# Kernel optimization log

Measured on AMD Instinct MI355X. Metric: run time of the kernel, lower is better.

## Reference

```python
import jax, jax.numpy as jnp
import numpy as np

B, L, D = 4, 4096, 128
BLOCK, SPARSITY = 64, 0.9
NEG = -1e9


def _make_block_mask(key):
    nb = L // BLOCK
    bm = jax.random.uniform(key, (nb, nb)) > SPARSITY
    bm = bm | jnp.eye(nb, dtype=bool)  # keep diagonal blocks so no row is fully masked
    bm = jnp.tril(bm)
    return jnp.repeat(jnp.repeat(bm, BLOCK, axis=0), BLOCK, axis=1)  # [L, L]


def _xavier(key, shape):
    limit = float(np.sqrt(6.0 / (shape[0] + shape[1])))
    return jax.random.uniform(key, shape, jnp.float32, -limit, limit)


def setup_inputs() -> dict:
    key = jax.random.key(0)
    ks = jax.random.split(key, 10)
    t = lambda k: jax.random.normal(k, (B, L, D), jnp.float32)
    return {
        'q_real': t(ks[0]), 'q_imag': t(ks[1]),
        'k_real': t(ks[2]), 'k_imag': t(ks[3]),
        'v_real': t(ks[4]), 'v_imag': t(ks[5]),
        'W_qkv': _xavier(ks[6], (6 * D, 6 * D)),
        'b_qkv': jnp.zeros((6 * D,), jnp.float32),
        'W_out': _xavier(ks[7], (2 * D, 2 * D)),
        'b_out': jnp.zeros((2 * D,), jnp.float32),
        'block_mask': _make_block_mask(ks[8]),
    }


def reference(q_real, q_imag, k_real, k_imag, v_real, v_imag,
              W_qkv, b_qkv, W_out, b_out, block_mask):
    d = q_real.shape[-1]
    scale = d ** -0.5
    # fused qkv projection over the 6 concatenated channels
    x = jnp.concatenate([q_real, q_imag, k_real, k_imag, v_real, v_imag], axis=-1)  # [B,L,6D]
    qkv = (x @ W_qkv.T + b_qkv).reshape(x.shape[0], x.shape[1], 6, d)
    q_r, q_i, k_r, k_i, v_r, v_i = (qkv[:, :, j] for j in range(6))

    def attn(q, k, v):
        s = jnp.einsum('bqd,bkd->bqk', q, k) * scale          # [B,L,L]
        s = jnp.where(block_mask[None], s, NEG)               # block-sparse mask
        a = jax.nn.softmax(s, axis=-1)                        # dropout = identity (eval)
        return jnp.einsum('bqk,bkd->bqd', a, v)

    out = jnp.concatenate([attn(q_r, k_r, v_r), attn(q_i, k_i, v_i)], axis=-1)  # [B,L,2D]
    out = out @ W_out.T + b_out
    return out[..., :d], out[..., d:]
```

## Files before the change

### kernel.cpp

```cpp
#include <hip/hip_runtime.h>
#include <hip/hip_bf16.h>

typedef unsigned short u16;
typedef __attribute__((ext_vector_type(8))) short bf16x8;
typedef __attribute__((ext_vector_type(4))) float f32x4;

#define SEQ_L 4096
#define M_TOT 16384

__device__ __forceinline__ float bf2f(u16 x) {
    unsigned u = ((unsigned)x) << 16;
    return __builtin_bit_cast(float, u);
}
__device__ __forceinline__ u16 f2bf(float f) {
    unsigned u = __builtin_bit_cast(unsigned, f);
    u += 0x7FFFu + ((u >> 16) & 1u);
    return (u16)(u >> 16);
}
__device__ __forceinline__ void gload16(const u16* g, u16* l) {
    __builtin_amdgcn_global_load_lds(
        (const __attribute__((address_space(1))) unsigned int*)g,
        (__attribute__((address_space(3))) unsigned int*)l, 16, 0, 0);
}

__global__ __launch_bounds__(256) void prep_all(
    const float* __restrict__ in0, const float* __restrict__ in1, const float* __restrict__ in2,
    const float* __restrict__ in3, const float* __restrict__ in4, const float* __restrict__ in5,
    const float* __restrict__ Wqkv, const float* __restrict__ Wout, const void* __restrict__ mask,
    u16* __restrict__ x, u16* __restrict__ Wqkv_bf, u16* __restrict__ Wout_bf,
    unsigned char* __restrict__ cmask) {
    int id = blockIdx.x * 256 + threadIdx.x;
    if (id < 1572864) {
        const float* ins[6] = {in0, in1, in2, in3, in4, in5};
        int which = id >> 18, j = id & 262143;
        int m = j >> 4, c8 = j & 15;
        const float* sp = ins[which] + (size_t)m * 128 + c8 * 8;
        float4 a = *(const float4*)sp;
        float4 b = *(const float4*)(sp + 4);
        u16 t[8] = {f2bf(a.x), f2bf(a.y), f2bf(a.z), f2bf(a.w),
                    f2bf(b.x), f2bf(b.y), f2bf(b.z), f2bf(b.w)};
        *(uint4*)(x + (size_t)m * 768 + which * 128 + c8 * 8) = *(uint4*)t;
    } else if (id < 1572864 + 73728 + 8192) {
        int i = id - 1572864;
        const float* src = (i < 73728) ? Wqkv : Wout;
        u16* dst = (i < 73728) ? Wqkv_bf : Wout_bf;
        if (i >= 73728) i -= 73728;
        const float* sp = src + (size_t)i * 8;
        float4 a = *(const float4*)sp;
        float4 b = *(const float4*)(sp + 4);
        u16 t[8] = {f2bf(a.x), f2bf(a.y), f2bf(a.z), f2bf(a.w),
                    f2bf(b.x), f2bf(b.y), f2bf(b.z), f2bf(b.w)};
        *(uint4*)(dst + (size_t)i * 8) = *(uint4*)t;
    } else if (id < 1572864 + 73728 + 8192 + 4096) {
        int i = id - 1572864 - 73728 - 8192;
        int bi = i >> 6, bj = i & 63;
        size_t e = (size_t)(bi * 64) * SEQ_L + (size_t)bj * 64;
        const unsigned char* p8 = (const unsigned char*)mask;
        unsigned w0 = *(const unsigned*)mask;
        bool v;
        if (w0 == 0x01010101u || w0 == 0xFFFFFFFFu)      v = p8[e] != 0;
        else if (w0 == 0x3F803F80u || w0 == 0x3C003C00u) v = ((const u16*)mask)[e] != 0;
        else                                             v = ((const unsigned*)mask)[e] != 0;
        cmask[i] = v ? 1 : 0;
    }
}

__global__ __launch_bounds__(256, 4) void qkv_gemm(
    const u16* __restrict__ X, const u16* __restrict__ W, const float* __restrict__ bias,
    u16* __restrict__ qk, u16* __restrict__ vt) {
    __shared__ __align__(16) u16 As[128 * 64];
    __shared__ __align__(16) u16 Bs[64 * 64];
    int m0 = blockIdx.x * 128, n0 = blockIdx.y * 64;
    int tid = threadIdx.x, lane = tid & 63, w = tid >> 6;
    int ln = lane & 15, quad = lane >> 4;
    int rw = (w >> 1) * 64, cw = (w & 1) * 32;
    int lr8 = lane >> 3, lc = lane & 7;
    f32x4 acc[4][2] = {};
    for (int kk = 0; kk < 768; kk += 64) {
        __syncthreads();
        #pragma unroll
        for (int j = 0; j < 4; j++) {
            int r0 = w * 32 + j * 8, r = r0 + lr8;
            gload16(X + (size_t)(m0 + r) * 768 + kk + ((lc ^ (r & 7)) * 8), As + r0 * 64 + lane * 8);
        }
        #pragma unroll
        for (int j = 0; j < 2; j++) {
            int r0 = w * 16 + j * 8, r = r0 + lr8;
            gload16(W + (size_t)(n0 + r) * 768 + kk + ((lc ^ (r & 7)) * 8), Bs + r0 * 64 + lane * 8);
        }
        __syncthreads();
        #pragma unroll
        for (int s = 0; s < 2; s++) {
            bf16x8 af[4], bfr[2];
            #pragma unroll
            for (int i = 0; i < 4; i++) {
                int R = rw + i * 16 + ln;
                af[i] = *(const bf16x8*)(As + R * 64 + ((4 * s + quad) ^ (ln & 7)) * 8);
            }
            #pragma unroll
            for (int t = 0; t < 2; t++) {
                int R = cw + t * 16 + ln;
                bfr[t] = *(const bf16x8*)(Bs + R * 64 + ((4 * s + quad) ^ (ln & 7)) * 8);
            }
            #pragma unroll
            for (int i = 0; i < 4; i++)
                #pragma unroll
                for (int t = 0; t < 2; t++)
                    acc[i][t] = __builtin_amdgcn_mfma_f32_16x16x32_bf16(af[i], bfr[t], acc[i][t], 0, 0, 0);
        }
    }
    #pragma unroll
    for (int i = 0; i < 4; i++) {
        int row0 = m0 + rw + i * 16 + 4 * quad;
        #pragma unroll
        for (int t = 0; t < 2; t++) {
            int col = n0 + cw + t * 16 + ln;
            float bv = bias[col];
            if (col < 512) {
                #pragma unroll
                for (int r = 0; r < 4; r++)
                    qk[(size_t)(row0 + r) * 512 + col] = f2bf(acc[i][t][r] + bv);
            } else {
                int d = col - 512;
                int b = row0 >> 12, seq = row0 & 4095;
                u16 pk[4] = {f2bf(acc[i][t][0] + bv), f2bf(acc[i][t][1] + bv),
                             f2bf(acc[i][t][2] + bv), f2bf(acc[i][t][3] + bv)};
                *(ushort4*)(vt + ((size_t)(b * 2 + (d >> 7)) * 128 + (d & 127)) * SEQ_L + seq)
                    = *(ushort4*)pk;
            }
        }
    }
}

__global__ __launch_bounds__(256) void attn_out(
    const u16* __restrict__ qk, const u16* __restrict__ vt, const u16* __restrict__ Wout,
    const unsigned char* __restrict__ cmask, const float* __restrict__ bout,
    float* __restrict__ out) {
    __shared__ __align__(16) u16 Ks[2][64 * 128];
    __shared__ __align__(16) u16 Vt[2][128 * 64];
    __shared__ __align__(16) u16 PsAo[32 * 256];

    int idx = blockIdx.x;
    int qi = (idx < 256) ? (63 - (idx >> 3)) : ((idx - 256) >> 3);
    int sub = idx & 7, b = sub >> 1, half = sub & 1;
    int tid = threadIdx.x, lane = tid & 63, w = tid >> 6;
    int ln = lane & 15, quad = lane >> 4;
    int cw = w >> 1, wr = w & 1;
    const float scale = 0.08838834764831845f;

    const unsigned char* mrow = cmask + qi * 64;
    unsigned long long bm = 0;
    for (int k = 0; k <= qi; k++) bm |= (unsigned long long)(mrow[k] != 0) << k;

    const u16* kb_base = qk + (size_t)b * SEQ_L * 512 + 256 + cw * 128;
    const u16* vt_base = vt + (size_t)(b * 2 + cw) * 128 * SEQ_L;

    bf16x8 qf[4];
    {
        size_t grow = (size_t)(b * SEQ_L + qi * 64 + half * 32 + wr * 16 + ln);
        const u16* qp = qk + grow * 512 + cw * 128;
        #pragma unroll
        for (int s = 0; s < 4; s++) qf[s] = *(const bf16x8*)(qp + 32 * s + 8 * quad);
    }
    float m_st[4], l_st[4];
    #pragma unroll
    for (int r = 0; r < 4; r++) { m_st[r] = -1e30f; l_st[r] = 0.f; }
    f32x4 accO[8] = {};
    u16* Ps = PsAo + w * 1152;

    while (bm) {
        int cur = __ffsll(bm) - 1; bm &= bm - 1;
        __syncthreads();
        {
            const u16* kp = kb_base + (size_t)cur * 64 * 512;
            const u16* vp = vt_base + cur * 64;
            #pragma unroll
            for (int j = 0; j < 8; j++) {
                int kr0 = j * 8 + wr * 4, kr = kr0 + (lane >> 4);
                gload16(kp + (size_t)kr * 512 + (((lane & 15) ^ (kr & 7)) * 8),
                        Ks[cw] + kr0 * 128 + lane * 8);
                int d0 = j * 16 + wr * 8, d = d0 + (lane >> 3);
                gload16(vp + (size_t)d * SEQ_L + (((lane & 7) ^ (d & 7)) * 8),
                        Vt[cw] + d0 * 64 + lane * 8);
            }
        }
        __syncthreads();

        f32x4 accS[4] = {};
        #pragma unroll
        for (int s = 0; s < 4; s++) {
            #pragma unroll
            for (int t = 0; t < 4; t++) {
                int R = t * 16 + ln;
                bf16x8 bfr = *(const bf16x8*)(Ks[cw] + R * 128 + ((4 * s + quad) ^ (ln & 7)) * 8);
                accS[t] = __builtin_amdgcn_mfma_f32_16x16x32_bf16(qf[s], bfr, accS[t], 0, 0, 0);
            }
        }
        float P[4][4];
        #pragma unroll
        for (int r = 0; r < 4; r++) {
            float sv[4];
            float mx = -1e30f;
            #pragma unroll
            for (int t = 0; t < 4; t++) { sv[t] = accS[t][r] * scale; mx = fmaxf(mx, sv[t]); }
            #pragma unroll
            for (int off = 1; off < 16; off <<= 1) mx = fmaxf(mx, __shfl_xor(mx, off, 64));
            float nm = fmaxf(m_st[r], mx);
            float alpha = __expf(m_st[r] - nm);
            m_st[r] = nm;
            float rs = 0.f;
            #pragma unroll
            for (int t = 0; t < 4; t++) { float p = __expf(sv[t] - nm); P[t][r] = p; rs += p; }
            #pragma unroll
            for (int off = 1; off < 16; off <<= 1) rs += __shfl_xor(rs, off, 64);
            l_st[r] = l_st[r] * alpha + rs;
            #pragma unroll
            for (int nt = 0; nt < 8; nt++) accO[nt][r] *= alpha;
        }
        #pragma unroll
        for (int t = 0; t < 4; t++)
            #pragma unroll
            for (int r = 0; r < 4; r++)
                Ps[(4 * quad + r) * 72 + ln + 16 * t] = f2bf(P[t][r]);
        #pragma unroll
        for (int s2 = 0; s2 < 2; s2++) {
            bf16x8 pf = *(const bf16x8*)(Ps + ln * 72 + 32 * s2 + 8 * quad);
            #pragma unroll
            for (int nt = 0; nt < 8; nt++) {
                int R = nt * 16 + ln;
                bf16x8 vf = *(const bf16x8*)(Vt[cw] + R * 64 + ((4 * s2 + quad) ^ (ln & 7)) * 8);
                accO[nt] = __builtin_amdgcn_mfma_f32_16x16x32_bf16(pf, vf, accO[nt], 0, 0, 0);
            }
        }
    }

    __syncthreads();
    {
        float inv[4];
        #pragma unroll
        for (int r = 0; r < 4; r++) inv[r] = 1.0f / fmaxf(l_st[r], 1e-20f);
        #pragma unroll
        for (int nt = 0; nt < 8; nt++)
            #pragma unroll
            for (int r = 0; r < 4; r++)
                PsAo[(wr * 16 + 4 * quad + r) * 256 + cw * 128 + nt * 16 + ln]
                    = f2bf(accO[nt][r] * inv[r]);
    }

    u16* Bs = Ks[0];
    f32x4 oacc[2][4] = {};
    for (int kk = 0; kk < 4; kk++) {
        __syncthreads();
        #pragma unroll
        for (int j = 0; j < 8; j++) {
            int o0 = w * 64 + j * 8, o = o0 + (lane >> 3);
            gload16(Wout + (size_t)o * 256 + kk * 64 + (((lane & 7) ^ (o & 7)) * 8),
                    Bs + o0 * 64 + lane * 8);
        }
        __syncthreads();
        #pragma unroll
        for (int s = 0; s < 2; s++) {
            bf16x8 af[2], bfr[4];
            #pragma unroll
            for (int i = 0; i < 2; i++)
                af[i] = *(const bf16x8*)(PsAo + (i * 16 + ln) * 256 + kk * 64 + 32 * s + 8 * quad);
            #pragma unroll
            for (int t = 0; t < 4; t++) {
                int o = w * 64 + t * 16 + ln;
                bfr[t] = *(const bf16x8*)(Bs + o * 64 + ((4 * s + quad) ^ (ln & 7)) * 8);
            }
            #pragma unroll
            for (int i = 0; i < 2; i++)
                #pragma unroll
                for (int t = 0; t < 4; t++)
                    oacc[i][t] = __builtin_amdgcn_mfma_f32_16x16x32_bf16(af[i], bfr[t], oacc[i][t], 0, 0, 0);
        }
    }
    const size_t hlf = (size_t)M_TOT * 128;
    #pragma unroll
    for (int t = 0; t < 4; t++) {
        int o = w * 64 + t * 16 + ln;
        float bv = bout[o];
        float* base = (o < 128) ? (out + o) : (out + hlf + (o - 128));
        #pragma unroll
        for (int i = 0; i < 2; i++) {
            int row = b * SEQ_L + qi * 64 + half * 32 + i * 16 + 4 * quad;
            #pragma unroll
            for (int r = 0; r < 4; r++)
                base[(size_t)(row + r) * 128] = oacc[i][t][r] + bv;
        }
    }
}

extern "C" void kernel_launch(void* const* d_in, const int* in_sizes, int n_in,
                              void* d_out, int out_size, void* d_ws, size_t ws_size,
                              hipStream_t stream) {
    char* ws = (char*)d_ws;
    u16* x_bf    = (u16*)ws;
    u16* qk_buf  = x_bf + (size_t)M_TOT * 768;
    u16* vt_buf  = qk_buf + (size_t)M_TOT * 512;
    u16* Wqkv_bf = vt_buf + (size_t)1024 * SEQ_L;
    u16* Wout_bf = Wqkv_bf + 589824;
    unsigned char* cmask = (unsigned char*)(Wout_bf + 65536);

    hipLaunchKernelGGL(prep_all, dim3(6480), dim3(256), 0, stream,
                       (const float*)d_in[0], (const float*)d_in[1], (const float*)d_in[2],
                       (const float*)d_in[3], (const float*)d_in[4], (const float*)d_in[5],
                       (const float*)d_in[6], (const float*)d_in[8], d_in[10],
                       x_bf, Wqkv_bf, Wout_bf, cmask);
    hipLaunchKernelGGL(qkv_gemm, dim3(128, 12), dim3(256), 0, stream,
                       x_bf, Wqkv_bf, (const float*)d_in[7], qk_buf, vt_buf);
    hipLaunchKernelGGL(attn_out, dim3(512), dim3(256), 0, stream,
                       qk_buf, vt_buf, Wout_bf, cmask, (const float*)d_in[9], (float*)d_out);
}
```

Baseline: 219.0 us.

## Split attention into wave-independent sparse kernel plus separate output GEMM

```diff
diff --git a/kernel.cpp b/kernel.cpp
--- a/kernel.cpp
+++ b/kernel.cpp
@@ -28,7 +28,7 @@
     const float* __restrict__ in3, const float* __restrict__ in4, const float* __restrict__ in5,
     const float* __restrict__ Wqkv, const float* __restrict__ Wout, const void* __restrict__ mask,
     u16* __restrict__ x, u16* __restrict__ Wqkv_bf, u16* __restrict__ Wout_bf,
-    unsigned char* __restrict__ cmask) {
+    unsigned long long* __restrict__ bmap) {
     int id = blockIdx.x * 256 + threadIdx.x;
     if (id < 1572864) {
         const float* ins[6] = {in0, in1, in2, in3, in4, in5};
@@ -61,7 +61,8 @@
         if (w0 == 0x01010101u || w0 == 0xFFFFFFFFu)      v = p8[e] != 0;
         else if (w0 == 0x3F803F80u || w0 == 0x3C003C00u) v = ((const u16*)mask)[e] != 0;
         else                                             v = ((const unsigned*)mask)[e] != 0;
-        cmask[i] = v ? 1 : 0;
+        unsigned long long bits = __ballot(v);
+        if ((i & 63) == 0) bmap[bi] = bits;
     }
 }
 
@@ -132,162 +133,156 @@
     }
 }
 
-__global__ __launch_bounds__(256) void attn_out(
-    const u16* __restrict__ qk, const u16* __restrict__ vt, const u16* __restrict__ Wout,
-    const unsigned char* __restrict__ cmask, const float* __restrict__ bout,
+__global__ __launch_bounds__(256, 2) void attn_sparse(
+    const u16* __restrict__ qk, const u16* __restrict__ vt,
+    const unsigned long long* __restrict__ bmap, u16* __restrict__ attn_bf) {
+    __shared__ __align__(16) u16 Ksm[4][32 * 128];
+    __shared__ __align__(16) u16 Vsm[4][128 * 32];
+    __shared__ __align__(16) u16 Psm[4][16 * 40];
+
+    int lane = threadIdx.x & 63, w = threadIdx.x >> 6;
+    int ln = lane & 15, quad = lane >> 4;
+    int g = blockIdx.x * 4 + w;
+    int u = g >> 5, v = g & 31;
+    int qi = (u < 32) ? (63 - u) : (u - 32);
+    int b = v >> 3, ch = (v >> 2) & 1, quarter = v & 3;
+    int rowbase = b * SEQ_L + qi * 64 + quarter * 16;
+    const float scale = 0.08838834764831845f;
+
+    u16* K = Ksm[w];
+    u16* V = Vsm[w];
+    u16* Ps = Psm[w];
+
+    bf16x8 qf[4];
+    {
+        const u16* qp = qk + (size_t)(rowbase + ln) * 512 + ch * 128;
+        #pragma unroll
+        for (int s = 0; s < 4; s++) qf[s] = *(const bf16x8*)(qp + 32 * s + 8 * quad);
+    }
+    float m_st[4], l_st[4];
+    #pragma unroll
+    for (int r = 0; r < 4; r++) { m_st[r] = -1e30f; l_st[r] = 0.f; }
+    f32x4 accO[8] = {};
+
+    const u16* kbase0 = qk + (size_t)b * SEQ_L * 512 + 256 + ch * 128;
+    const u16* vbase0 = vt + (size_t)(b * 2 + ch) * 128 * SEQ_L;
+    unsigned long long bm = bmap[qi];
+
+    while (bm) {
+        int kb = __ffsll(bm) - 1; bm &= bm - 1;
+        #pragma unroll
+        for (int sub = 0; sub < 2; sub++) {
+            const u16* kp = kbase0 + (size_t)(kb * 64 + sub * 32) * 512;
+            const u16* vp = vbase0 + kb * 64 + sub * 32;
+            #pragma unroll
+            for (int j = 0; j < 8; j++) {
+                int kr = j * 4 + (lane >> 4);
+                gload16(kp + (size_t)kr * 512 + (((lane & 15) ^ (kr & 7)) * 8),
+                        K + j * 4 * 128 + lane * 8);
+            }
+            #pragma unroll
+            for (int j = 0; j < 8; j++) {
+                int d = j * 16 + (lane >> 2);
+                gload16(vp + (size_t)d * SEQ_L + (((lane & 3) ^ (d & 3)) * 8),
+                        V + j * 16 * 32 + lane * 8);
+            }
+            __builtin_amdgcn_s_waitcnt(0x0F78);
+
+            f32x4 accS[2] = {};
+            #pragma unroll
+            for (int s = 0; s < 4; s++)
+                #pragma unroll
+                for (int t = 0; t < 2; t++) {
+                    bf16x8 kf = *(const bf16x8*)(K + (t * 16 + ln) * 128 +
+                                                 (((4 * s + quad) ^ (ln & 7)) * 8));
+                    accS[t] = __builtin_amdgcn_mfma_f32_16x16x32_bf16(qf[s], kf, accS[t], 0, 0, 0);
+                }
+
+            #pragma unroll
+            for (int r = 0; r < 4; r++) {
+                float s0 = accS[0][r] * scale, s1 = accS[1][r] * scale;
+                float mx = fmaxf(s0, s1);
+                #pragma unroll
+                for (int off = 1; off < 16; off <<= 1) mx = fmaxf(mx, __shfl_xor(mx, off, 64));
+                float nm = fmaxf(m_st[r], mx);
+                float alpha = __expf(m_st[r] - nm);
+                m_st[r] = nm;
+                float p0 = __expf(s0 - nm), p1 = __expf(s1 - nm);
+                Ps[(4 * quad + r) * 40 + ln] = f2bf(p0);
+                Ps[(4 * quad + r) * 40 + ln + 16] = f2bf(p1);
+                float rs = p0 + p1;
+                #pragma unroll
+                for (int off = 1; off < 16; off <<= 1) rs += __shfl_xor(rs, off, 64);
+                l_st[r] = l_st[r] * alpha + rs;
+                #pragma unroll
+                for (int nt = 0; nt < 8; nt++) accO[nt][r] *= alpha;
+            }
+
+            __builtin_amdgcn_s_waitcnt(0x0F70);
+            bf16x8 pf = *(const bf16x8*)(Ps + ln * 40 + 8 * quad);
+            #pragma unroll
+            for (int nt = 0; nt < 8; nt++) {
+                bf16x8 vf = *(const bf16x8*)(V + (nt * 16 + ln) * 32 +
+                                             ((quad ^ (ln & 3)) * 8));
+                accO[nt] = __builtin_amdgcn_mfma_f32_16x16x32_bf16(pf, vf, accO[nt], 0, 0, 0);
+            }
+        }
+    }
+
+    float inv[4];
+    #pragma unroll
+    for (int r = 0; r < 4; r++) inv[r] = 1.0f / fmaxf(l_st[r], 1e-20f);
+    #pragma unroll
+    for (int nt = 0; nt < 8; nt++)
+        #pragma unroll
+        for (int r = 0; r < 4; r++)
+            attn_bf[(size_t)(rowbase + 4 * quad + r) * 256 + ch * 128 + nt * 16 + ln]
+                = f2bf(accO[nt][r] * inv[r]);
+}
+
+__global__ __launch_bounds__(256) void out_gemm(
+    const u16* __restrict__ A, const u16* __restrict__ W, const float* __restrict__ bias,
     float* __restrict__ out) {
-    __shared__ __align__(16) u16 Ks[2][64 * 128];
-    __shared__ __align__(16) u16 Vt[2][128 * 64];
-    __shared__ __align__(16) u16 PsAo[32 * 256];
-
-    int idx = blockIdx.x;
-    int qi = (idx < 256) ? (63 - (idx >> 3)) : ((idx - 256) >> 3);
-    int sub = idx & 7, b = sub >> 1, half = sub & 1;
+    __shared__ __align__(16) u16 As[64 * 64];
+    __shared__ __align__(16) u16 Bs[64 * 64];
+    int m0 = blockIdx.x * 64, n0 = blockIdx.y * 64;
     int tid = threadIdx.x, lane = tid & 63, w = tid >> 6;
     int ln = lane & 15, quad = lane >> 4;
-    int cw = w >> 1, wr = w & 1;
-    const float scale = 0.08838834764831845f;
-
-    const unsigned char* mrow = cmask + qi * 64;
-    unsigned long long bm = 0;
-    for (int k = 0; k <= qi; k++) bm |= (unsigned long long)(mrow[k] != 0) << k;
-
-    const u16* kb_base = qk + (size_t)b * SEQ_L * 512 + 256 + cw * 128;
-    const u16* vt_base = vt + (size_t)(b * 2 + cw) * 128 * SEQ_L;
-
-    bf16x8 qf[4];
-    {
-        size_t grow = (size_t)(b * SEQ_L + qi * 64 + half * 32 + wr * 16 + ln);
-        const u16* qp = qk + grow * 512 + cw * 128;
-        #pragma unroll
-        for (int s = 0; s < 4; s++) qf[s] = *(const bf16x8*)(qp + 32 * s + 8 * quad);
-    }
-    float m_st[4], l_st[4];
-    #pragma unroll
-    for (int r = 0; r < 4; r++) { m_st[r] = -1e30f; l_st[r] = 0.f; }
-    f32x4 accO[8] = {};
-    u16* Ps = PsAo + w * 1152;
-
-    while (bm) {
-        int cur = __ffsll(bm) - 1; bm &= bm - 1;
+    int lr8 = lane >> 3, lc = lane & 7;
+    int swz_st = lc ^ (lr8 & 7);
+    f32x4 acc[4] = {};
+    for (int kk = 0; kk < 256; kk += 64) {
         __syncthreads();
-        {
-            const u16* kp = kb_base + (size_t)cur * 64 * 512;
-            const u16* vp = vt_base + cur * 64;
-            #pragma unroll
-            for (int j = 0; j < 8; j++) {
-                int kr0 = j * 8 + wr * 4, kr = kr0 + (lane >> 4);
-                gload16(kp + (size_t)kr * 512 + (((lane & 15) ^ (kr & 7)) * 8),
-                        Ks[cw] + kr0 * 128 + lane * 8);
-                int d0 = j * 16 + wr * 8, d = d0 + (lane >> 3);
-                gload16(vp + (size_t)d * SEQ_L + (((lane & 7) ^ (d & 7)) * 8),
-                        Vt[cw] + d0 * 64 + lane * 8);
-            }
+        #pragma unroll
+        for (int j = 0; j < 2; j++) {
+            int r0 = w * 16 + j * 8;
+            int r = r0 + lr8;
+            gload16(A + (size_t)(m0 + r) * 256 + kk + swz_st * 8, As + r0 * 64 + lane * 8);
+            gload16(W + (size_t)(n0 + r) * 256 + kk + swz_st * 8, Bs + r0 * 64 + lane * 8);
         }
         __syncthreads();
-
-        f32x4 accS[4] = {};
-        #pragma unroll
-        for (int s = 0; s < 4; s++) {
+        #pragma unroll
+        for (int s = 0; s < 2; s++) {
+            int R = w * 16 + ln;
+            bf16x8 af = *(const bf16x8*)(As + R * 64 + ((4 * s + quad) ^ (ln & 7)) * 8);
             #pragma unroll
             for (int t = 0; t < 4; t++) {
-                int R = t * 16 + ln;
-                bf16x8 bfr = *(const bf16x8*)(Ks[cw] + R * 128 + ((4 * s + quad) ^ (ln & 7)) * 8);
-                accS[t] = __builtin_amdgcn_mfma_f32_16x16x32_bf16(qf[s], bfr, accS[t], 0, 0, 0);
-            }
-        }
-        float P[4][4];
+                int Rb = t * 16 + ln;
+                bf16x8 bfr = *(const bf16x8*)(Bs + Rb * 64 + ((4 * s + quad) ^ (ln & 7)) * 8);
+                acc[t] = __builtin_amdgcn_mfma_f32_16x16x32_bf16(af, bfr, acc[t], 0, 0, 0);
+            }
+        }
+    }
+    const size_t half = (size_t)M_TOT * 128;
+    #pragma unroll
+    for (int t = 0; t < 4; t++) {
+        int col = n0 + t * 16 + ln;
+        float bv = bias[col];
+        float* base = (col < 128) ? (out + col) : (out + half + (col - 128));
         #pragma unroll
         for (int r = 0; r < 4; r++) {
-            float sv[4];
-            float mx = -1e30f;
-            #pragma unroll
-            for (int t = 0; t < 4; t++) { sv[t] = accS[t][r] * scale; mx = fmaxf(mx, sv[t]); }
-            #pragma unroll
-            for (int off = 1; off < 16; off <<= 1) mx = fmaxf(mx, __shfl_xor(mx, off, 64));
-            float nm = fmaxf(m_st[r], mx);
-            float alpha = __expf(m_st[r] - nm);
-            m_st[r] = nm;
-            float rs = 0.f;
-            #pragma unroll
-            for (int t = 0; t < 4; t++) { float p = __expf(sv[t] - nm); P[t][r] = p; rs += p; }
-            #pragma unroll
-            for (int off = 1; off < 16; off <<= 1) rs += __shfl_xor(rs, off, 64);
-            l_st[r] = l_st[r] * alpha + rs;
-            #pragma unroll
-            for (int nt = 0; nt < 8; nt++) accO[nt][r] *= alpha;
-        }
-        #pragma unroll
-        for (int t = 0; t < 4; t++)
-            #pragma unroll
-            for (int r = 0; r < 4; r++)
-                Ps[(4 * quad + r) * 72 + ln + 16 * t] = f2bf(P[t][r]);
-        #pragma unroll
-        for (int s2 = 0; s2 < 2; s2++) {
-            bf16x8 pf = *(const bf16x8*)(Ps + ln * 72 + 32 * s2 + 8 * quad);
-            #pragma unroll
-            for (int nt = 0; nt < 8; nt++) {
-                int R = nt * 16 + ln;
-                bf16x8 vf = *(const bf16x8*)(Vt[cw] + R * 64 + ((4 * s2 + quad) ^ (ln & 7)) * 8);
-                accO[nt] = __builtin_amdgcn_mfma_f32_16x16x32_bf16(pf, vf, accO[nt], 0, 0, 0);
-            }
-        }
-    }
-
-    __syncthreads();
-    {
-        float inv[4];
-        #pragma unroll
-        for (int r = 0; r < 4; r++) inv[r] = 1.0f / fmaxf(l_st[r], 1e-20f);
-        #pragma unroll
-        for (int nt = 0; nt < 8; nt++)
-            #pragma unroll
-            for (int r = 0; r < 4; r++)
-                PsAo[(wr * 16 + 4 * quad + r) * 256 + cw * 128 + nt * 16 + ln]
-                    = f2bf(accO[nt][r] * inv[r]);
-    }
-
-    u16* Bs = Ks[0];
-    f32x4 oacc[2][4] = {};
-    for (int kk = 0; kk < 4; kk++) {
-        __syncthreads();
-        #pragma unroll
-        for (int j = 0; j < 8; j++) {
-            int o0 = w * 64 + j * 8, o = o0 + (lane >> 3);
-            gload16(Wout + (size_t)o * 256 + kk * 64 + (((lane & 7) ^ (o & 7)) * 8),
-                    Bs + o0 * 64 + lane * 8);
-        }
-        __syncthreads();
-        #pragma unroll
-        for (int s = 0; s < 2; s++) {
-            bf16x8 af[2], bfr[4];
-            #pragma unroll
-            for (int i = 0; i < 2; i++)
-                af[i] = *(const bf16x8*)(PsAo + (i * 16 + ln) * 256 + kk * 64 + 32 * s + 8 * quad);
-            #pragma unroll
-            for (int t = 0; t < 4; t++) {
-                int o = w * 64 + t * 16 + ln;
-                bfr[t] = *(const bf16x8*)(Bs + o * 64 + ((4 * s + quad) ^ (ln & 7)) * 8);
-            }
-            #pragma unroll
-            for (int i = 0; i < 2; i++)
-                #pragma unroll
-                for (int t = 0; t < 4; t++)
-                    oacc[i][t] = __builtin_amdgcn_mfma_f32_16x16x32_bf16(af[i], bfr[t], oacc[i][t], 0, 0, 0);
-        }
-    }
-    const size_t hlf = (size_t)M_TOT * 128;
-    #pragma unroll
-    for (int t = 0; t < 4; t++) {
-        int o = w * 64 + t * 16 + ln;
-        float bv = bout[o];
-        float* base = (o < 128) ? (out + o) : (out + hlf + (o - 128));
-        #pragma unroll
-        for (int i = 0; i < 2; i++) {
-            int row = b * SEQ_L + qi * 64 + half * 32 + i * 16 + 4 * quad;
-            #pragma unroll
-            for (int r = 0; r < 4; r++)
-                base[(size_t)(row + r) * 128] = oacc[i][t][r] + bv;
+            int row = m0 + w * 16 + 4 * quad + r;
+            base[(size_t)row * 128] = acc[t][r] + bv;
         }
     }
 }
@@ -299,17 +294,20 @@
     u16* x_bf    = (u16*)ws;
     u16* qk_buf  = x_bf + (size_t)M_TOT * 768;
     u16* vt_buf  = qk_buf + (size_t)M_TOT * 512;
-    u16* Wqkv_bf = vt_buf + (size_t)1024 * SEQ_L;
+    u16* attn_bf = vt_buf + (size_t)1024 * SEQ_L;
+    u16* Wqkv_bf = attn_bf + (size_t)M_TOT * 256;
     u16* Wout_bf = Wqkv_bf + 589824;
-    unsigned char* cmask = (unsigned char*)(Wout_bf + 65536);
+    unsigned long long* bmap = (unsigned long long*)(Wout_bf + 65536);
 
     hipLaunchKernelGGL(prep_all, dim3(6480), dim3(256), 0, stream,
                        (const float*)d_in[0], (const float*)d_in[1], (const float*)d_in[2],
                        (const float*)d_in[3], (const float*)d_in[4], (const float*)d_in[5],
                        (const float*)d_in[6], (const float*)d_in[8], d_in[10],
-                       x_bf, Wqkv_bf, Wout_bf, cmask);
+                       x_bf, Wqkv_bf, Wout_bf, bmap);
     hipLaunchKernelGGL(qkv_gemm, dim3(128, 12), dim3(256), 0, stream,
                        x_bf, Wqkv_bf, (const float*)d_in[7], qk_buf, vt_buf);
-    hipLaunchKernelGGL(attn_out, dim3(512), dim3(256), 0, stream,
-                       qk_buf, vt_buf, Wout_bf, cmask, (const float*)d_in[9], (float*)d_out);
-}
+    hipLaunchKernelGGL(attn_sparse, dim3(512), dim3(256), 0, stream,
+                       qk_buf, vt_buf, bmap, attn_bf);
+    hipLaunchKernelGGL(out_gemm, dim3(256, 4), dim3(256), 0, stream,
+                       attn_bf, Wout_bf, (const float*)d_in[9], (float*)d_out);
+}
```

Result: no change. 216.7 us (-1.1%).
